# Kernel optimization log

Hardware: AMD Instinct MI355X
Metric: run time of the kernel (lower is better)

The kernel has to match this reference:

```python
import jax, jax.numpy as jnp
import numpy as np

B, I, N, D, C = 1024, 256, 2048, 32, 32  # batch, input channels, nodes, node out dim, node fan-in


def setup_inputs() -> dict:
    key = jax.random.key(0)
    ks = jax.random.split(key, 8)
    x = jax.random.normal(ks[0], (B, I), jnp.float32)
    h0 = jnp.zeros((B, N, D), jnp.float32)            # previous-step hidden state per node
    conv_w = jax.random.normal(ks[1], (I,), jnp.float32)   # Conv1d(I,I,1,groups=I) weight
    conv_b = jax.random.normal(ks[2], (I,), jnp.float32)
    W = jax.random.normal(ks[3], (N, D, C), jnp.float32) * 0.1  # per-node Linear(C->D)
    b = jax.random.normal(ks[4], (N, D), jnp.float32) * 0.1
    W_out = jax.random.normal(ks[5], (1, C), jnp.float32) * 0.1  # Layers[-2]: Linear(C->1)
    b_out = jax.random.normal(ks[6], (1,), jnp.float32) * 0.1
    # flat gather index into concat([relu-conv input (I), h_flat (N*D)], axis=1)
    idx = jax.random.randint(ks[7], (N, C), 0, I + N * D, jnp.int32)
    return {"x": x, "h0": h0, "conv_w": conv_w, "conv_b": conv_b,
            "W": W, "b": b, "W_out": W_out, "b_out": b_out, "idx": idx}


def reference(x, h0, conv_w, conv_b, W, b, W_out, b_out, idx):
    # trace[-1] = ReLU(depthwise 1x1 conv) == per-channel affine
    inp = jax.nn.relu(x * conv_w + conv_b)                      # (B, I)
    # cross-node reads come from previous h (detached state), so all nodes
    # can be computed in one vectorized gather + batched small GEMM.
    buf = jnp.concatenate([inp, h0.reshape(B, N * D)], axis=1)  # (B, I+N*D)
    gathered = buf[:, idx]                                      # (B, N, C) irregular gather
    out_nodes = jax.nn.relu(jnp.einsum('bnc,ndc->bnd', gathered, W) + b)  # (B, N, D)
    last_in = gathered[:, -1]                                   # tensor_in of last node (B, C)
    out2 = jax.nn.relu(last_in @ W_out.T + b_out)               # trace[-2], (B, 1)
    return out_nodes[:, -1], out2
```

## Files before the change

### kernel.cpp

```cpp
#include <hip/hip_runtime.h>

#define B_ 1024
#define I_ 256
#define N_ 2048
#define D_ 32
#define C_ 32

__global__ __launch_bounds__(256) void prnn_last_kernel(
    const float* __restrict__ x, const float* __restrict__ h0,
    const float* __restrict__ conv_w, const float* __restrict__ conv_b,
    const float* __restrict__ W, const float* __restrict__ bvec,
    const float* __restrict__ W_out, const float* __restrict__ b_out,
    const int* __restrict__ idx,
    float* __restrict__ out_nodes, float* __restrict__ out2)
{
    __shared__ float Ws[D_][C_ + 1];
    __shared__ float gs[8][C_];
    __shared__ float bs[D_];
    __shared__ float wouts[C_];
    __shared__ int   idxs[C_];

    const int tid = threadIdx.x;

    for (int t = tid; t < D_ * C_; t += 256) {
        Ws[t / C_][t % C_] = W[(size_t)(N_ - 1) * D_ * C_ + t];
    }
    if (tid < D_) bs[tid] = bvec[(size_t)(N_ - 1) * D_ + tid];
    if (tid < C_) { wouts[tid] = W_out[tid]; idxs[tid] = idx[(size_t)(N_ - 1) * C_ + tid]; }
    __syncthreads();

    const int row = tid >> 5;
    const int lane = tid & 31;
    const int b = blockIdx.x * 8 + row;

    {
        const int j = idxs[lane];
        float v;
        if (j < I_) {
            v = fmaf(x[(size_t)b * I_ + j], conv_w[j], conv_b[j]);
            v = v > 0.f ? v : 0.f;
        } else {
            v = h0[(size_t)b * (N_ * D_) + (size_t)(j - I_)];
        }
        gs[row][lane] = v;
    }
    __syncthreads();

    float acc = bs[lane];
    #pragma unroll
    for (int c = 0; c < C_; ++c) acc = fmaf(gs[row][c], Ws[lane][c], acc);
    acc = acc > 0.f ? acc : 0.f;
    out_nodes[(size_t)b * D_ + lane] = acc;

    if (lane == 0) {
        float a2 = b_out[0];
        #pragma unroll
        for (int c = 0; c < C_; ++c) a2 = fmaf(gs[row][c], wouts[c], a2);
        out2[b] = a2 > 0.f ? a2 : 0.f;
    }
}

extern "C" void kernel_launch(void* const* d_in, const int* in_sizes, int n_in,
                              void* d_out, int out_size, void* d_ws, size_t ws_size,
                              hipStream_t stream) {
    const float* x      = (const float*)d_in[0];
    const float* h0     = (const float*)d_in[1];
    const float* conv_w = (const float*)d_in[2];
    const float* conv_b = (const float*)d_in[3];
    const float* W      = (const float*)d_in[4];
    const float* bvec   = (const float*)d_in[5];
    const float* W_out  = (const float*)d_in[6];
    const float* b_out  = (const float*)d_in[7];
    const int*   idx    = (const int*)d_in[8];

    float* out       = (float*)d_out;
    float* out2      = out + (size_t)B_ * D_;

    prnn_last_kernel<<<B_ / 8, 256, 0, stream>>>(
        x, h0, conv_w, conv_b, W, bvec, W_out, b_out, idx, out, out2);
}
```

Baseline: 9.748 us.

## Replace shared-memory staging with register weights and warp shuffles

Drops the shared-memory staging of W, bias, idx and the gathered row, along with both __syncthreads barriers. Each lane now loads its own W row into registers with float4 loads and broadcasts the gathered values across the 32-lane group with __shfl. The out2 dot product becomes a butterfly shuffle reduction instead of a serial loop on lane 0. The cost is more global and L2 traffic, since every 32-lane group reloads the 4KB W tile, and about 32 extra registers per thread.

```diff
diff --git a/kernel.cpp b/kernel.cpp
--- a/kernel.cpp
+++ b/kernel.cpp
@@ -14,50 +14,41 @@
     const int* __restrict__ idx,
     float* __restrict__ out_nodes, float* __restrict__ out2)
 {
-    __shared__ float Ws[D_][C_ + 1];
-    __shared__ float gs[8][C_];
-    __shared__ float bs[D_];
-    __shared__ float wouts[C_];
-    __shared__ int   idxs[C_];
+    const int tid  = threadIdx.x;
+    const int row  = tid >> 5;
+    const int lane = tid & 31;
+    const int b    = blockIdx.x * 8 + row;
 
-    const int tid = threadIdx.x;
+    const int j = idx[(size_t)(N_ - 1) * C_ + lane];
+    float g;
+    if (j < I_) {
+        float v = fmaf(x[(size_t)b * I_ + j], conv_w[j], conv_b[j]);
+        g = v > 0.f ? v : 0.f;
+    } else {
+        g = h0[(size_t)b * (N_ * D_) + (size_t)(j - I_)];
+    }
 
-    for (int t = tid; t < D_ * C_; t += 256) {
-        Ws[t / C_][t % C_] = W[(size_t)(N_ - 1) * D_ * C_ + t];
+    float wr[C_];
+    const float* Wrow = W + (size_t)(N_ - 1) * D_ * C_ + (size_t)lane * C_;
+    #pragma unroll
+    for (int q = 0; q < C_ / 4; ++q) {
+        float4 v = reinterpret_cast<const float4*>(Wrow)[q];
+        wr[4 * q + 0] = v.x; wr[4 * q + 1] = v.y;
+        wr[4 * q + 2] = v.z; wr[4 * q + 3] = v.w;
     }
-    if (tid < D_) bs[tid] = bvec[(size_t)(N_ - 1) * D_ + tid];
-    if (tid < C_) { wouts[tid] = W_out[tid]; idxs[tid] = idx[(size_t)(N_ - 1) * C_ + tid]; }
-    __syncthreads();
+    float acc  = bvec[(size_t)(N_ - 1) * D_ + lane];
+    float wout = W_out[lane];
+    float bo   = b_out[0];
 
-    const int row = tid >> 5;
-    const int lane = tid & 31;
-    const int b = blockIdx.x * 8 + row;
+    #pragma unroll
+    for (int c = 0; c < C_; ++c)
+        acc = fmaf(__shfl(g, c, 32), wr[c], acc);
+    out_nodes[(size_t)b * D_ + lane] = acc > 0.f ? acc : 0.f;
 
-    {
-        const int j = idxs[lane];
-        float v;
-        if (j < I_) {
-            v = fmaf(x[(size_t)b * I_ + j], conv_w[j], conv_b[j]);
-            v = v > 0.f ? v : 0.f;
-        } else {
-            v = h0[(size_t)b * (N_ * D_) + (size_t)(j - I_)];
-        }
-        gs[row][lane] = v;
-    }
-    __syncthreads();
-
-    float acc = bs[lane];
+    float p = g * wout;
     #pragma unroll
-    for (int c = 0; c < C_; ++c) acc = fmaf(gs[row][c], Ws[lane][c], acc);
-    acc = acc > 0.f ? acc : 0.f;
-    out_nodes[(size_t)b * D_ + lane] = acc;
-
-    if (lane == 0) {
-        float a2 = b_out[0];
-        #pragma unroll
-        for (int c = 0; c < C_; ++c) a2 = fmaf(gs[row][c], wouts[c], a2);
-        out2[b] = a2 > 0.f ? a2 : 0.f;
-    }
+    for (int m = 16; m; m >>= 1) p += __shfl_xor(p, m, 32);
+    if (lane == 0) out2[b] = fmaxf(p + bo, 0.f);
 }
 
 extern "C" void kernel_launch(void* const* d_in, const int* in_sizes, int n_in,
@@ -73,8 +64,8 @@
     const float* b_out  = (const float*)d_in[7];
     const int*   idx    = (const int*)d_in[8];
 
-    float* out       = (float*)d_out;
-    float* out2      = out + (size_t)B_ * D_;
+    float* out  = (float*)d_out;
+    float* out2 = out + (size_t)B_ * D_;
 
     prnn_last_kernel<<<B_ / 8, 256, 0, stream>>>(
         x, h0, conv_w, conv_b, W, bvec, W_out, b_out, idx, out, out2);
```

Result: no change. 9.709 us (-0.4%).
